# Optimization experiments

Measured on AMD Instinct MI355X. Metric: run time of the kernel, lower is better.

Reference implementation:

```python
import jax, jax.numpy as jnp
import numpy as np

B, T, D, H, C = 256, 512, 300, 128, 6

def setup_inputs() -> dict:
    key = jax.random.key(0)
    ks = jax.random.split(key, 8)
    s = 1.0 / np.sqrt(H)  # PyTorch LSTM/Linear uniform init scale
    x = jax.random.normal(ks[0], (B, T, D), dtype=jnp.float32)
    lengths = jax.random.randint(ks[1], (B,), 1, T + 1)
    W_ih = jax.random.uniform(ks[2], (4 * H, D), minval=-s, maxval=s, dtype=jnp.float32)
    W_hh = jax.random.uniform(ks[3], (4 * H, H), minval=-s, maxval=s, dtype=jnp.float32)
    b_ih = jax.random.uniform(ks[4], (4 * H,), minval=-s, maxval=s, dtype=jnp.float32)
    b_hh = jax.random.uniform(ks[5], (4 * H,), minval=-s, maxval=s, dtype=jnp.float32)
    fc_w = jax.random.uniform(ks[6], (C, H), minval=-s, maxval=s, dtype=jnp.float32)
    fc_b = jax.random.uniform(ks[7], (C,), minval=-s, maxval=s, dtype=jnp.float32)
    return {"x": x, "W_ih": W_ih, "W_hh": W_hh, "b_ih": b_ih, "b_hh": b_hh,
            "fc_w": fc_w, "fc_b": fc_b, "lengths": lengths}

def _lstm_last_hidden(x, W_ih, W_hh, b_ih, b_hh, lengths):
    # Equivalent to pack_padded_sequence + nn.LSTM: the returned hidden[-1]
    # is the state at t = length-1 for each sequence. We run a masked scan:
    # state updates are frozen once t >= length.
    Bv, Tv, _ = x.shape
    Hv = W_hh.shape[1]
    xs = jnp.swapaxes(x, 0, 1)                              # [T, B, D]
    gx = jnp.einsum('tbd,gd->tbg', xs, W_ih) + b_ih + b_hh  # [T, B, 4H]
    mask = (jnp.arange(Tv)[:, None] < lengths[None, :])     # [T, B]

    def step(carry, inp):
        h, c = carry
        g, m = inp
        gates = g + h @ W_hh.T                              # [B, 4H]
        i, f, gg, o = jnp.split(gates, 4, axis=-1)          # PyTorch gate order i,f,g,o
        i = jax.nn.sigmoid(i)
        f = jax.nn.sigmoid(f)
        gg = jnp.tanh(gg)
        o = jax.nn.sigmoid(o)
        c_new = f * c + i * gg
        h_new = o * jnp.tanh(c_new)
        m = m[:, None]
        h = jnp.where(m, h_new, h)
        c = jnp.where(m, c_new, c)
        return (h, c), None

    h0 = jnp.zeros((Bv, Hv), dtype=x.dtype)
    c0 = jnp.zeros((Bv, Hv), dtype=x.dtype)
    (h, c), _ = jax.lax.scan(step, (h0, c0), (gx, mask))
    return h

def reference(x, W_ih, W_hh, b_ih, b_hh, fc_w, fc_b, lengths):
    h = _lstm_last_hidden(x, W_ih, W_hh, b_ih, b_hh, lengths)  # [B, H]
    return h @ fc_w.T + fc_b                                   # [B, 6]
```

## Files before the change

kernel.cpp:

```cpp
#include <hip/hip_runtime.h>
#include <hip/hip_bf16.h>
#include <stdint.h>
#include <type_traits>

#define NB 256
#define NT 512
#define ND 300
#define NH 128
#define NG 512
#define NC 6

typedef __attribute__((ext_vector_type(8))) short short8;
typedef __attribute__((ext_vector_type(4))) float f32x4;

static __device__ __forceinline__ float bf2f(unsigned int u) {
  return __builtin_bit_cast(float, (u & 0xffffu) << 16);
}
static __device__ __forceinline__ unsigned short f2bf(float f) {
  return __builtin_bit_cast(unsigned short, __float2bfloat16(f));
}
static __device__ __forceinline__ unsigned int packbf(float a, float b) {
  return (unsigned int)f2bf(a) | ((unsigned int)f2bf(b) << 16);
}
static __device__ __forceinline__ float ld1(const unsigned short* p) { return bf2f(*p); }
static __device__ __forceinline__ float ld1(const float* p) { return *p; }
static __device__ __forceinline__ void st1(unsigned short* p, float v) { *p = f2bf(v); }
static __device__ __forceinline__ void st1(float* p, float v) { *p = v; }

static __device__ __forceinline__ float sigmoid_fast(float x) {
  return __builtin_amdgcn_rcpf(1.f + __expf(-x));
}
static __device__ __forceinline__ float tanh_fast(float x) {
  return 1.f - 2.f * __builtin_amdgcn_rcpf(__expf(2.f * x) + 1.f);
}

#define BARRIER_LGKM() asm volatile("s_waitcnt lgkmcnt(0)\n\ts_barrier" ::: "memory")

static __device__ __forceinline__ uint2 load4bf_fast(const unsigned short* row, int k) {
  return *(const uint2*)(row + k);
}
static __device__ __forceinline__ uint2 load4bf_fast(const float* row, int k) {
  float4 f = *(const float4*)(row + k);
  uint2 v;
  v.x = packbf(f.x, f.y);
  v.y = packbf(f.z, f.w);
  return v;
}
static __device__ __forceinline__ uint2 load4bf(const unsigned short* row, int k, int lim) {
  if (k + 3 < lim) return load4bf_fast(row, k);
  unsigned int e0 = (k + 0 < lim) ? row[k + 0] : 0;
  unsigned int e1 = (k + 1 < lim) ? row[k + 1] : 0;
  unsigned int e2 = (k + 2 < lim) ? row[k + 2] : 0;
  unsigned int e3 = (k + 3 < lim) ? row[k + 3] : 0;
  uint2 v;
  v.x = e0 | (e1 << 16);
  v.y = e2 | (e3 << 16);
  return v;
}
static __device__ __forceinline__ uint2 load4bf(const float* row, int k, int lim) {
  if (k + 3 < lim) return load4bf_fast(row, k);
  float f0 = (k + 0 < lim) ? row[k + 0] : 0.f;
  float f1 = (k + 1 < lim) ? row[k + 1] : 0.f;
  float f2 = (k + 2 < lim) ? row[k + 2] : 0.f;
  float f3 = (k + 3 < lim) ? row[k + 3] : 0.f;
  uint2 v;
  v.x = packbf(f0, f1);
  v.y = packbf(f2, f3);
  return v;
}

static __device__ __forceinline__ int block_detect(const unsigned short* __restrict__ X,
                                                   int* cnt) {
  const int tid = threadIdx.x;
  const int nthr = blockDim.x;
  if (tid == 0) *cnt = 0;
  __syncthreads();
  int c = 0;
  for (int i = tid; i < 512; i += nthr) {
    unsigned int u = X[i];
    unsigned int e = (u >> 7) & 0xffu;
    if (u == 0u || (e >= 97u && e <= 157u)) c++;
  }
  if (c) atomicAdd(cnt, c);
  __syncthreads();
  return (*cnt >= 448) ? 0 : 1;
}

template <typename XT, typename GXT>
static __device__ __forceinline__ void gx_body(
    const XT* __restrict__ X, const XT* __restrict__ Wih,
    const XT* __restrict__ bih, const XT* __restrict__ bhh,
    const int* __restrict__ lengths, GXT* __restrict__ gx,
    int b_base, int t_base, int Tc, unsigned short* smem) {
  auto As = reinterpret_cast<unsigned short(*)[64][40]>(smem);
  auto Bs = reinterpret_cast<unsigned short(*)[128][40]>(smem + 25600);

  const int mb = blockIdx.x;
  const int m0 = mb << 6;
  const int bc = m0 / Tc;
  const int trel0 = m0 % Tc;
  const int b = b_base + bc;
  const int t0 = t_base + trel0;
  const int len = lengths[b];
  if (t0 >= len) return;

  const int tid = threadIdx.x;
  const int lane = tid & 63;
  const int wave = tid >> 6;
  const int wm = wave & 1;
  const int wn = wave >> 1;
  const int lq = lane >> 4;
  const int lr = lane & 15;

  const int rA = tid >> 2;
  const int cA = (tid & 3) << 2;
  const XT* xrow = X + ((size_t)b * NT + t0 + rA) * ND;
  {
    uint2 a0[10], a1[10];
#pragma unroll
    for (int kc = 0; kc < 9; ++kc) {
      a0[kc] = load4bf_fast(xrow, kc * 32 + cA);
      a1[kc] = load4bf_fast(xrow, kc * 32 + 16 + cA);
    }
    a0[9] = load4bf(xrow, 288 + cA, ND);
    a1[9] = load4bf(xrow, 288 + 16 + cA, ND);
#pragma unroll
    for (int kc = 0; kc < 10; ++kc) {
      *(uint2*)&As[kc][rA][cA] = a0[kc];
      *(uint2*)&As[kc][rA][16 + cA] = a1[kc];
    }
  }

  const int rb = tid >> 3;
  const int kq = tid & 7;

  uint2 bv[3][4];
  {
    const XT* wb = Wih + (size_t)rb * ND;
#pragma unroll
    for (int s3 = 0; s3 < 3; ++s3)
#pragma unroll
      for (int j = 0; j < 4; ++j)
        bv[s3][j] = load4bf_fast(wb + (size_t)(32 * j) * ND, s3 * 32 + kq * 4);
  }

  for (int nt = 0; nt < 4; ++nt) {
    const int n0 = nt << 7;
    const XT* wb = Wih + (size_t)(n0 + rb) * ND;

    f32x4 acc[2][4];
#pragma unroll
    for (int i = 0; i < 2; ++i)
#pragma unroll
      for (int j = 0; j < 4; ++j) {
        f32x4 z = {0.f, 0.f, 0.f, 0.f};
        acc[i][j] = z;
      }

#pragma unroll
    for (int j = 0; j < 4; ++j) *(uint2*)&Bs[0][rb + 32 * j][kq * 4] = bv[0][j];
    BARRIER_LGKM();

#pragma unroll
    for (int kc = 0; kc < 10; ++kc) {
      const int bi = kc & 1;
      if (kc < 9) {
#pragma unroll
        for (int j = 0; j < 4; ++j)
          *(uint2*)&Bs[bi ^ 1][rb + 32 * j][kq * 4] = bv[(kc + 1) % 3][j];
      }
      if (kc < 7) {
        const int kn = (kc + 3) * 32 + kq * 4;
        if (kc < 6) {
#pragma unroll
          for (int j = 0; j < 4; ++j)
            bv[kc % 3][j] = load4bf_fast(wb + (size_t)(32 * j) * ND, kn);
        } else {
#pragma unroll
          for (int j = 0; j < 4; ++j)
            bv[kc % 3][j] = load4bf(wb + (size_t)(32 * j) * ND, kn, ND);
        }
      }

      short8 af[2], bq[4];
#pragma unroll
      for (int tm = 0; tm < 2; ++tm)
        af[tm] = *(const short8*)&As[kc][wm * 32 + tm * 16 + lr][lq * 8];
#pragma unroll
      for (int tn = 0; tn < 4; ++tn)
        bq[tn] = *(const short8*)&Bs[bi][wn * 64 + tn * 16 + lr][lq * 8];
#pragma unroll
      for (int tm = 0; tm < 2; ++tm)
#pragma unroll
        for (int tn = 0; tn < 4; ++tn)
          acc[tm][tn] =
              __builtin_amdgcn_mfma_f32_16x16x32_bf16(af[tm], bq[tn], acc[tm][tn], 0, 0, 0);
      BARRIER_LGKM();
    }

    if (nt < 3) {
      const XT* wb2 = Wih + (size_t)((nt + 1) * 128 + rb) * ND;
#pragma unroll
      for (int s3 = 0; s3 < 3; ++s3)
#pragma unroll
        for (int j = 0; j < 4; ++j)
          bv[s3][j] = load4bf_fast(wb2 + (size_t)(32 * j) * ND, s3 * 32 + kq * 4);
    }

    float bias_c[4];
#pragma unroll
    for (int tn = 0; tn < 4; ++tn) {
      const int col = n0 + wn * 64 + tn * 16 + lr;
      bias_c[tn] = ld1(bih + col) + ld1(bhh + col);
    }
#pragma unroll
    for (int tm = 0; tm < 2; ++tm)
#pragma unroll
      for (int tn = 0; tn < 4; ++tn)
#pragma unroll
        for (int rg = 0; rg < 4; ++rg) {
          const int row = wm * 32 + tm * 16 + lq * 4 + rg;
          if (t0 + row < len) {
            const int col = n0 + wn * 64 + tn * 16 + lr;
            st1(gx + (size_t)(m0 + row) * NG + col, acc[tm][tn][rg] + bias_c[tn]);
          }
        }
  }
}

template <typename XT, typename GXT>
static __device__ __forceinline__ void rec_body(
    const GXT* __restrict__ gx, const XT* __restrict__ Whh,
    const XT* __restrict__ fcw, const XT* __restrict__ fcb,
    const int* __restrict__ lengths, XT* __restrict__ out,
    float* __restrict__ hstate, float* __restrict__ cstate,
    int b_base, int t_base, int Tc,
    unsigned short (*hpk)[NH], float* hf) {
  const int bc = blockIdx.x;
  const int b = b_base + bc;
  int len = lengths[b];
  if (len > NT) len = NT;
  if (len < 0) len = 0;
  const bool first = (t_base == 0);
  const bool last = (t_base + Tc >= NT);
  const int tend = (len < t_base + Tc) ? len : (t_base + Tc);
  if (!last && tend <= t_base) return;
  int nsteps = tend - t_base;
  if (nsteps < 0) nsteps = 0;

  const int tid = threadIdx.x;
  const int w8 = tid >> 6;
  const int l = tid & 63;
  const int q = l >> 4;
  const int m = l & 15;
  const int u0 = w8 * 16 + q * 4;
  const int r = m & 3;
  const int u = u0 + r;

  short8 afr[4][4];
#pragma unroll
  for (int g = 0; g < 4; ++g) {
    const int row = g * NH + w8 * 16 + m;
    if constexpr (std::is_same_v<XT, unsigned short>) {
#pragma unroll
      for (int c = 0; c < 4; ++c)
        afr[g][c] = *(const short8*)(Whh + (size_t)row * NH + c * 32 + q * 8);
    } else {
#pragma unroll
      for (int c = 0; c < 4; ++c) {
        const float* p = Whh + (size_t)row * NH + c * 32 + q * 8;
        float4 f0 = *(const float4*)p;
        float4 f1 = *(const float4*)(p + 4);
        union { unsigned int uu[4]; short8 s; } cv2;
        cv2.uu[0] = packbf(f0.x, f0.y);
        cv2.uu[1] = packbf(f0.z, f0.w);
        cv2.uu[2] = packbf(f1.x, f1.y);
        cv2.uu[3] = packbf(f1.z, f1.w);
        afr[g][c] = cv2.s;
      }
    }
  }

  float hcur = 0.f, ccur = 0.f;
  if (!first) {
    hcur = hstate[(size_t)bc * NH + u];
    ccur = cstate[(size_t)bc * NH + u];
  }
  if (m < 4) hpk[0][u] = f2bf(hcur);
  __syncthreads();

  const GXT* gp = gx + (size_t)bc * Tc * NG + u;
  const int lastidx = (nsteps > 0) ? nsteps - 1 : 0;

  float gs0[4], gs1[4];
  {
    const int i1 = (1 < lastidx) ? 1 : lastidx;
#pragma unroll
    for (int g = 0; g < 4; ++g) {
      gs0[g] = ld1(gp + g * NH);
      gs1[g] = ld1(gp + (size_t)i1 * NG + g * NH);
    }
  }

#define REC_STEP(S, PAR, GC)                                                         \
  {                                                                                  \
    short8 bfr[4];                                                                   \
    const unsigned short* hrow = hpk[(PAR)];                                         \
    _Pragma("unroll") for (int c = 0; c < 4; ++c)                                    \
        bfr[c] = *(const short8*)&hrow[c * 32 + q * 8];                              \
    const f32x4 zz = {0.f, 0.f, 0.f, 0.f};                                           \
    f32x4 acc[4];                                                                    \
    _Pragma("unroll") for (int g = 0; g < 4; ++g) {                                  \
      f32x4 p0 = __builtin_amdgcn_mfma_f32_16x16x32_bf16(afr[g][0], bfr[0], zz, 0, 0, 0); \
      f32x4 p1 = __builtin_amdgcn_mfma_f32_16x16x32_bf16(afr[g][1], bfr[1], zz, 0, 0, 0); \
      f32x4 p2 = __builtin_amdgcn_mfma_f32_16x16x32_bf16(afr[g][2], bfr[2], zz, 0, 0, 0); \
      f32x4 p3 = __builtin_amdgcn_mfma_f32_16x16x32_bf16(afr[g][3], bfr[3], zz, 0, 0, 0); \
      acc[g] = (p0 + p1) + (p2 + p3);                                                \
    }                                                                                \
    float pre[4];                                                                    \
    _Pragma("unroll") for (int g = 0; g < 4; ++g) {                                  \
      const float t0v = (r & 1) ? acc[g][1] : acc[g][0];                             \
      const float t1v = (r & 1) ? acc[g][3] : acc[g][2];                             \
      pre[g] = ((r & 2) ? t1v : t0v) + GC[g];                                        \
    }                                                                                \
    {                                                                                \
      int idx_ = (S) + 2;                                                            \
      if (idx_ > lastidx) idx_ = lastidx;                                            \
      _Pragma("unroll") for (int g = 0; g < 4; ++g)                                  \
          GC[g] = ld1(gp + (size_t)idx_ * NG + g * NH);                              \
    }                                                                                \
    const float ig = sigmoid_fast(pre[0]);                                           \
    const float fg = sigmoid_fast(pre[1]);                                           \
    const float gg = tanh_fast(pre[2]);                                              \
    const float og = sigmoid_fast(pre[3]);                                           \
    ccur = fmaf(fg, ccur, ig * gg);                                                  \
    hcur = og * tanh_fast(ccur);                                                     \
    if (m < 4) hpk[(PAR) ^ 1][u] = f2bf(hcur);                                       \
    BARRIER_LGKM();                                                                  \
  }

  int s = 0;
  for (; s + 1 < nsteps; s += 2) {
    REC_STEP(s, 0, gs0);
    REC_STEP(s + 1, 1, gs1);
  }
  if (s < nsteps) {
    REC_STEP(s, 0, gs0);
  }
#undef REC_STEP

  if (!last) {
    if (m < 4) {
      hstate[(size_t)bc * NH + u] = hcur;
      cstate[(size_t)bc * NH + u] = ccur;
    }
  } else {
    if (m < 4) hf[u] = hcur;
    __syncthreads();
    if (tid < NC) {
      float acc = ld1(fcb + tid);
      const XT* wv = fcw + (size_t)tid * NH;
#pragma unroll
      for (int k = 0; k < NH; ++k) acc = fmaf(ld1(wv + k), hf[k], acc);
      st1(out + (size_t)b * NC + tid, acc);
    }
  }
}

template <typename GXT>
__global__ __launch_bounds__(256) void gx_gemm_rt(const void* __restrict__ X,
                                                  const void* __restrict__ Wih,
                                                  const void* __restrict__ bih,
                                                  const void* __restrict__ bhh,
                                                  const int* __restrict__ lengths,
                                                  GXT* __restrict__ gx,
                                                  int b_base, int t_base, int Tc) {
  __shared__ int cnt;
  __shared__ __align__(16) unsigned short smem[35840];
  const int isf32 = block_detect((const unsigned short*)X, &cnt);
  if (isf32)
    gx_body<float, GXT>((const float*)X, (const float*)Wih, (const float*)bih,
                        (const float*)bhh, lengths, gx, b_base, t_base, Tc, smem);
  else
    gx_body<unsigned short, GXT>((const unsigned short*)X, (const unsigned short*)Wih,
                                 (const unsigned short*)bih, (const unsigned short*)bhh,
                                 lengths, gx, b_base, t_base, Tc, smem);
}

template <typename GXT>
__global__ __launch_bounds__(512)
__attribute__((amdgpu_waves_per_eu(2, 2)))
void lstm_rec_rt(const void* __restrict__ X, const GXT* __restrict__ gx,
                 const void* __restrict__ Whh, const void* __restrict__ fcw,
                 const void* __restrict__ fcb, const int* __restrict__ lengths,
                 void* __restrict__ out, float* __restrict__ hstate,
                 float* __restrict__ cstate, int b_base, int t_base, int Tc) {
  __shared__ int cnt;
  __shared__ __align__(16) unsigned short hpk[2][NH];
  __shared__ __align__(16) float hf[NH];
  const int isf32 = block_detect((const unsigned short*)X, &cnt);
  if (isf32)
    rec_body<float, GXT>(gx, (const float*)Whh, (const float*)fcw, (const float*)fcb,
                         lengths, (float*)out, hstate, cstate, b_base, t_base, Tc,
                         hpk, hf);
  else
    rec_body<unsigned short, GXT>(gx, (const unsigned short*)Whh,
                                  (const unsigned short*)fcw,
                                  (const unsigned short*)fcb, lengths,
                                  (unsigned short*)out, hstate, cstate, b_base,
                                  t_base, Tc, hpk, hf);
}

template <typename GXT>
static void run_all(void* const* d_in, void* d_out, GXT* gx, float* hstate,
                    float* cstate, int NBc, int Tc, hipStream_t stream) {
  const int* lengths = (const int*)d_in[7];
  for (int bb = 0; bb < NB; bb += NBc) {
    for (int tb = 0; tb < NT; tb += Tc) {
      gx_gemm_rt<GXT><<<dim3((NBc * Tc) / 64), dim3(256), 0, stream>>>(
          d_in[0], d_in[1], d_in[3], d_in[4], lengths, gx, bb, tb, Tc);
      lstm_rec_rt<GXT><<<dim3(NBc), dim3(512), 0, stream>>>(
          d_in[0], gx, d_in[2], d_in[5], d_in[6], lengths, d_out, hstate, cstate,
          bb, tb, Tc);
    }
  }
}

extern "C" void kernel_launch(void* const* d_in, const int* in_sizes, int n_in,
                              void* d_out, int out_size, void* d_ws, size_t ws_size,
                              hipStream_t stream) {
  const size_t full_f32 = (size_t)NB * NT * NG * sizeof(float);
  const size_t full_bf16 = (size_t)NB * NT * NG * 2;
  const size_t base = 512;

  int NBc, Tc;
  char* gx_raw;
  float* hstate = (float*)((char*)d_ws + base);
  bool gx_is_f32;

  if (ws_size >= base + full_f32) {
    NBc = NB; Tc = NT; gx_is_f32 = true;
    gx_raw = (char*)d_ws + base;
  } else if (ws_size >= base + full_bf16) {
    NBc = NB; Tc = NT; gx_is_f32 = false;
    gx_raw = (char*)d_ws + base;
  } else {
    Tc = 128; gx_is_f32 = false;
    NBc = 1;
    for (int cand : {64, 16, 4}) {
      size_t need = base + (size_t)cand * NH * 2 * sizeof(float) + (size_t)cand * Tc * NG * 2;
      if (ws_size >= need) { NBc = cand; break; }
    }
    gx_raw = (char*)d_ws + base + (size_t)NBc * NH * 2 * sizeof(float);
  }
  float* cstate = hstate + (size_t)NBc * NH;

  if (gx_is_f32) {
    run_all<float>(d_in, d_out, (float*)gx_raw, hstate, cstate, NBc, Tc, stream);
  } else {
    run_all<unsigned short>(d_in, d_out, (unsigned short*)gx_raw, hstate, cstate,
                            NBc, Tc, stream);
  }
}
```

Measured before the change: 710.3 us.

## Widen gx GEMM blocks to 512 threads with transposed MFMA and vectorized stores

The input-projection GEMM now runs with 512 threads per block, each wave covering a 32x32 output tile instead of 32x64. Operands are swapped in the MFMA so each lane holds four consecutive gate columns, which lets the epilogue write gx as one 16-byte (or packed bf16) store instead of scalar stores. The recurrent step drops the four partial-sum MFMAs plus adds in favour of a chained accumulation. This aims for better memory coalescing and latency hiding in the GEMM, at the cost of more per-block register and barrier pressure and a longer MFMA dependency chain in the recurrence.

```diff
diff --git a/kernel.cpp b/kernel.cpp
--- a/kernel.cpp
+++ b/kernel.cpp
@@ -87,144 +87,194 @@
 }
 
 template <typename XT, typename GXT>
-static __device__ __forceinline__ void gx_body(
+static __device__ __forceinline__ void gx_prod(
     const XT* __restrict__ X, const XT* __restrict__ Wih,
     const XT* __restrict__ bih, const XT* __restrict__ bhh,
-    const int* __restrict__ lengths, GXT* __restrict__ gx,
-    int b_base, int t_base, int Tc, unsigned short* smem) {
+    int b, int t0, int len, GXT* __restrict__ gxrow, unsigned short* smem) {
   auto As = reinterpret_cast<unsigned short(*)[64][40]>(smem);
   auto Bs = reinterpret_cast<unsigned short(*)[128][40]>(smem + 25600);
-
-  const int mb = blockIdx.x;
-  const int m0 = mb << 6;
-  const int bc = m0 / Tc;
-  const int trel0 = m0 % Tc;
-  const int b = b_base + bc;
-  const int t0 = t_base + trel0;
-  const int len = lengths[b];
-  if (t0 >= len) return;
 
   const int tid = threadIdx.x;
   const int lane = tid & 63;
   const int wave = tid >> 6;
-  const int wm = wave & 1;
-  const int wn = wave >> 1;
+  const int wt = wave & 1;
+  const int wn4 = wave >> 1;
   const int lq = lane >> 4;
   const int lr = lane & 15;
 
-  const int rA = tid >> 2;
-  const int cA = (tid & 3) << 2;
+  const int rA = tid >> 3;
+  const int cA = (tid & 7) << 2;
   const XT* xrow = X + ((size_t)b * NT + t0 + rA) * ND;
   {
-    uint2 a0[10], a1[10];
-#pragma unroll
-    for (int kc = 0; kc < 9; ++kc) {
-      a0[kc] = load4bf_fast(xrow, kc * 32 + cA);
-      a1[kc] = load4bf_fast(xrow, kc * 32 + 16 + cA);
-    }
-    a0[9] = load4bf(xrow, 288 + cA, ND);
-    a1[9] = load4bf(xrow, 288 + 16 + cA, ND);
-#pragma unroll
-    for (int kc = 0; kc < 10; ++kc) {
-      *(uint2*)&As[kc][rA][cA] = a0[kc];
-      *(uint2*)&As[kc][rA][16 + cA] = a1[kc];
-    }
-  }
-
-  const int rb = tid >> 3;
-  const int kq = tid & 7;
-
-  uint2 bv[3][4];
+    uint2 a[10];
+#pragma unroll
+    for (int kc = 0; kc < 9; ++kc) a[kc] = load4bf_fast(xrow, kc * 32 + cA);
+    a[9] = load4bf(xrow, 288 + cA, ND);
+#pragma unroll
+    for (int kc = 0; kc < 10; ++kc) *(uint2*)&As[kc][rA][cA] = a[kc];
+  }
+
+  const int rb = tid >> 2;
+  const int kqo = (tid & 3) << 3;
+  uint2 bv[3][2];
   {
     const XT* wb = Wih + (size_t)rb * ND;
 #pragma unroll
-    for (int s3 = 0; s3 < 3; ++s3)
-#pragma unroll
-      for (int j = 0; j < 4; ++j)
-        bv[s3][j] = load4bf_fast(wb + (size_t)(32 * j) * ND, s3 * 32 + kq * 4);
+    for (int s3 = 0; s3 < 3; ++s3) {
+      bv[s3][0] = load4bf_fast(wb, s3 * 32 + kqo);
+      bv[s3][1] = load4bf_fast(wb, s3 * 32 + kqo + 4);
+    }
   }
 
   for (int nt = 0; nt < 4; ++nt) {
     const int n0 = nt << 7;
     const XT* wb = Wih + (size_t)(n0 + rb) * ND;
 
-    f32x4 acc[2][4];
+    f32x4 acc[2][2];
 #pragma unroll
     for (int i = 0; i < 2; ++i)
 #pragma unroll
-      for (int j = 0; j < 4; ++j) {
+      for (int j = 0; j < 2; ++j) {
         f32x4 z = {0.f, 0.f, 0.f, 0.f};
         acc[i][j] = z;
       }
 
-#pragma unroll
-    for (int j = 0; j < 4; ++j) *(uint2*)&Bs[0][rb + 32 * j][kq * 4] = bv[0][j];
+    *(uint2*)&Bs[0][rb][kqo] = bv[0][0];
+    *(uint2*)&Bs[0][rb][kqo + 4] = bv[0][1];
     BARRIER_LGKM();
 
 #pragma unroll
     for (int kc = 0; kc < 10; ++kc) {
       const int bi = kc & 1;
       if (kc < 9) {
-#pragma unroll
-        for (int j = 0; j < 4; ++j)
-          *(uint2*)&Bs[bi ^ 1][rb + 32 * j][kq * 4] = bv[(kc + 1) % 3][j];
+        *(uint2*)&Bs[bi ^ 1][rb][kqo] = bv[(kc + 1) % 3][0];
+        *(uint2*)&Bs[bi ^ 1][rb][kqo + 4] = bv[(kc + 1) % 3][1];
       }
       if (kc < 7) {
-        const int kn = (kc + 3) * 32 + kq * 4;
+        const int kn = (kc + 3) * 32 + kqo;
         if (kc < 6) {
-#pragma unroll
-          for (int j = 0; j < 4; ++j)
-            bv[kc % 3][j] = load4bf_fast(wb + (size_t)(32 * j) * ND, kn);
+          bv[kc % 3][0] = load4bf_fast(wb, kn);
+          bv[kc % 3][1] = load4bf_fast(wb, kn + 4);
         } else {
-#pragma unroll
-          for (int j = 0; j < 4; ++j)
-            bv[kc % 3][j] = load4bf(wb + (size_t)(32 * j) * ND, kn, ND);
+          bv[kc % 3][0] = load4bf(wb, kn, ND);
+          bv[kc % 3][1] = load4bf(wb, kn + 4, ND);
         }
       }
 
-      short8 af[2], bq[4];
-#pragma unroll
-      for (int tm = 0; tm < 2; ++tm)
-        af[tm] = *(const short8*)&As[kc][wm * 32 + tm * 16 + lr][lq * 8];
-#pragma unroll
-      for (int tn = 0; tn < 4; ++tn)
-        bq[tn] = *(const short8*)&Bs[bi][wn * 64 + tn * 16 + lr][lq * 8];
-#pragma unroll
-      for (int tm = 0; tm < 2; ++tm)
-#pragma unroll
-        for (int tn = 0; tn < 4; ++tn)
-          acc[tm][tn] =
-              __builtin_amdgcn_mfma_f32_16x16x32_bf16(af[tm], bq[tn], acc[tm][tn], 0, 0, 0);
+      short8 wF[2], aX[2];
+#pragma unroll
+      for (int tn = 0; tn < 2; ++tn)
+        wF[tn] = *(const short8*)&Bs[bi][wn4 * 32 + tn * 16 + lr][lq * 8];
+#pragma unroll
+      for (int tt = 0; tt < 2; ++tt)
+        aX[tt] = *(const short8*)&As[kc][wt * 32 + tt * 16 + lr][lq * 8];
+#pragma unroll
+      for (int tt = 0; tt < 2; ++tt)
+#pragma unroll
+        for (int tn = 0; tn < 2; ++tn)
+          acc[tt][tn] =
+              __builtin_amdgcn_mfma_f32_16x16x32_bf16(wF[tn], aX[tt], acc[tt][tn], 0, 0, 0);
       BARRIER_LGKM();
     }
 
     if (nt < 3) {
       const XT* wb2 = Wih + (size_t)((nt + 1) * 128 + rb) * ND;
 #pragma unroll
-      for (int s3 = 0; s3 < 3; ++s3)
-#pragma unroll
-        for (int j = 0; j < 4; ++j)
-          bv[s3][j] = load4bf_fast(wb2 + (size_t)(32 * j) * ND, s3 * 32 + kq * 4);
-    }
-
-    float bias_c[4];
-#pragma unroll
-    for (int tn = 0; tn < 4; ++tn) {
-      const int col = n0 + wn * 64 + tn * 16 + lr;
-      bias_c[tn] = ld1(bih + col) + ld1(bhh + col);
-    }
-#pragma unroll
-    for (int tm = 0; tm < 2; ++tm)
-#pragma unroll
-      for (int tn = 0; tn < 4; ++tn)
-#pragma unroll
-        for (int rg = 0; rg < 4; ++rg) {
-          const int row = wm * 32 + tm * 16 + lq * 4 + rg;
-          if (t0 + row < len) {
-            const int col = n0 + wn * 64 + tn * 16 + lr;
-            st1(gx + (size_t)(m0 + row) * NG + col, acc[tm][tn][rg] + bias_c[tn]);
+      for (int s3 = 0; s3 < 3; ++s3) {
+        bv[s3][0] = load4bf_fast(wb2, s3 * 32 + kqo);
+        bv[s3][1] = load4bf_fast(wb2, s3 * 32 + kqo + 4);
+      }
+    }
+
+    f32x4 bias4[2];
+#pragma unroll
+    for (int tn = 0; tn < 2; ++tn) {
+      const int n = n0 + wn4 * 32 + tn * 16 + lq * 4;
+#pragma unroll
+      for (int rg = 0; rg < 4; ++rg) bias4[tn][rg] = ld1(bih + n + rg) + ld1(bhh + n + rg);
+    }
+#pragma unroll
+    for (int tt = 0; tt < 2; ++tt) {
+      const int trow = wt * 32 + tt * 16 + lr;
+      if (t0 + trow < len) {
+#pragma unroll
+        for (int tn = 0; tn < 2; ++tn) {
+          const int n = n0 + wn4 * 32 + tn * 16 + lq * 4;
+          f32x4 o = acc[tt][tn] + bias4[tn];
+          if constexpr (std::is_same_v<GXT, float>) {
+            *(f32x4*)(gxrow + (size_t)trow * NG + n) = o;
+          } else {
+            uint2 v;
+            v.x = packbf(o[0], o[1]);
+            v.y = packbf(o[2], o[3]);
+            *(uint2*)(gxrow + (size_t)trow * NG + n) = v;
           }
         }
+      }
+    }
+  }
+}
+
+#define REC_STEP(S, PAR, GC, CAP)                                                    \
+  {                                                                                  \
+    short8 bfr[4];                                                                   \
+    const unsigned short* hrow = hpk[(PAR)];                                         \
+    _Pragma("unroll") for (int c = 0; c < 4; ++c)                                    \
+        bfr[c] = *(const short8*)&hrow[c * 32 + q * 8];                              \
+    f32x4 acc[4];                                                                    \
+    _Pragma("unroll") for (int g = 0; g < 4; ++g) {                                  \
+      f32x4 z = {0.f, 0.f, 0.f, 0.f};                                                \
+      acc[g] = z;                                                                    \
+      _Pragma("unroll") for (int c = 0; c < 4; ++c)                                  \
+          acc[g] = __builtin_amdgcn_mfma_f32_16x16x32_bf16(afr[g][c], bfr[c],        \
+                                                           acc[g], 0, 0, 0);         \
+    }                                                                                \
+    float pre[4];                                                                    \
+    _Pragma("unroll") for (int g = 0; g < 4; ++g) {                                  \
+      const float t0v = (r & 1) ? acc[g][1] : acc[g][0];                             \
+      const float t1v = (r & 1) ? acc[g][3] : acc[g][2];                             \
+      pre[g] = ((r & 2) ? t1v : t0v) + GC[g];                                        \
+    }                                                                                \
+    {                                                                                \
+      int idx_ = (S) + 2;                                                            \
+      if (idx_ > (CAP)) idx_ = (CAP);                                                \
+      _Pragma("unroll") for (int g = 0; g < 4; ++g)                                  \
+          GC[g] = ld1(gp + (size_t)idx_ * NG + g * NH);                              \
+    }                                                                                \
+    const float ig = sigmoid_fast(pre[0]);                                           \
+    const float fg = sigmoid_fast(pre[1]);                                           \
+    const float gg = tanh_fast(pre[2]);                                              \
+    const float og = sigmoid_fast(pre[3]);                                           \
+    ccur = fmaf(fg, ccur, ig * gg);                                                  \
+    hcur = og * tanh_fast(ccur);                                                     \
+    if (m < 4) hpk[(PAR) ^ 1][u] = f2bf(hcur);                                       \
+    BARRIER_LGKM();                                                                  \
+  }
+
+template <typename XT>
+static __device__ __forceinline__ void load_afr(const XT* __restrict__ Whh, int w8,
+                                                int q, int m, short8 afr[4][4]) {
+#pragma unroll
+  for (int g = 0; g < 4; ++g) {
+    const int row = g * NH + w8 * 16 + m;
+    if constexpr (std::is_same_v<XT, unsigned short>) {
+#pragma unroll
+      for (int c = 0; c < 4; ++c)
+        afr[g][c] = *(const short8*)(Whh + (size_t)row * NH + c * 32 + q * 8);
+    } else {
+#pragma unroll
+      for (int c = 0; c < 4; ++c) {
+        const float* p = Whh + (size_t)row * NH + c * 32 + q * 8;
+        float4 f0 = *(const float4*)p;
+        float4 f1 = *(const float4*)(p + 4);
+        union { unsigned int uu[4]; short8 s; } cv2;
+        cv2.uu[0] = packbf(f0.x, f0.y);
+        cv2.uu[1] = packbf(f0.z, f0.w);
+        cv2.uu[2] = packbf(f1.x, f1.y);
+        cv2.uu[3] = packbf(f1.z, f1.w);
+        afr[g][c] = cv2.s;
+      }
+    }
   }
 }
 
@@ -258,28 +308,7 @@
   const int u = u0 + r;
 
   short8 afr[4][4];
-#pragma unroll
-  for (int g = 0; g < 4; ++g) {
-    const int row = g * NH + w8 * 16 + m;
-    if constexpr (std::is_same_v<XT, unsigned short>) {
-#pragma unroll
-      for (int c = 0; c < 4; ++c)
-        afr[g][c] = *(const short8*)(Whh + (size_t)row * NH + c * 32 + q * 8);
-    } else {
-#pragma unroll
-      for (int c = 0; c < 4; ++c) {
-        const float* p = Whh + (size_t)row * NH + c * 32 + q * 8;
-        float4 f0 = *(const float4*)p;
-        float4 f1 = *(const float4*)(p + 4);
-        union { unsigned int uu[4]; short8 s; } cv2;
-        cv2.uu[0] = packbf(f0.x, f0.y);
-        cv2.uu[1] = packbf(f0.z, f0.w);
-        cv2.uu[2] = packbf(f1.x, f1.y);
-        cv2.uu[3] = packbf(f1.z, f1.w);
-        afr[g][c] = cv2.s;
-      }
-    }
-  }
+  load_afr<XT>(Whh, w8, q, m, afr);
 
   float hcur = 0.f, ccur = 0.f;
   if (!first) {
@@ -302,52 +331,14 @@
     }
   }
 
-#define REC_STEP(S, PAR, GC)                                                         \
-  {                                                                                  \
-    short8 bfr[4];                                                                   \
-    const unsigned short* hrow = hpk[(PAR)];                                         \
-    _Pragma("unroll") for (int c = 0; c < 4; ++c)                                    \
-        bfr[c] = *(const short8*)&hrow[c * 32 + q * 8];                              \
-    const f32x4 zz = {0.f, 0.f, 0.f, 0.f};                                           \
-    f32x4 acc[4];                                                                    \
-    _Pragma("unroll") for (int g = 0; g < 4; ++g) {                                  \
-      f32x4 p0 = __builtin_amdgcn_mfma_f32_16x16x32_bf16(afr[g][0], bfr[0], zz, 0, 0, 0); \
-      f32x4 p1 = __builtin_amdgcn_mfma_f32_16x16x32_bf16(afr[g][1], bfr[1], zz, 0, 0, 0); \
-      f32x4 p2 = __builtin_amdgcn_mfma_f32_16x16x32_bf16(afr[g][2], bfr[2], zz, 0, 0, 0); \
-      f32x4 p3 = __builtin_amdgcn_mfma_f32_16x16x32_bf16(afr[g][3], bfr[3], zz, 0, 0, 0); \
-      acc[g] = (p0 + p1) + (p2 + p3);                                                \
-    }                                                                                \
-    float pre[4];                                                                    \
-    _Pragma("unroll") for (int g = 0; g < 4; ++g) {                                  \
-      const float t0v = (r & 1) ? acc[g][1] : acc[g][0];                             \
-      const float t1v = (r & 1) ? acc[g][3] : acc[g][2];                             \
-      pre[g] = ((r & 2) ? t1v : t0v) + GC[g];                                        \
-    }                                                                                \
-    {                                                                                \
-      int idx_ = (S) + 2;                                                            \
-      if (idx_ > lastidx) idx_ = lastidx;                                            \
-      _Pragma("unroll") for (int g = 0; g < 4; ++g)                                  \
-          GC[g] = ld1(gp + (size_t)idx_ * NG + g * NH);                              \
-    }                                                                                \
-    const float ig = sigmoid_fast(pre[0]);                                           \
-    const float fg = sigmoid_fast(pre[1]);                                           \
-    const float gg = tanh_fast(pre[2]);                                              \
-    const float og = sigmoid_fast(pre[3]);                                           \
-    ccur = fmaf(fg, ccur, ig * gg);                                                  \
-    hcur = og * tanh_fast(ccur);                                                     \
-    if (m < 4) hpk[(PAR) ^ 1][u] = f2bf(hcur);                                       \
-    BARRIER_LGKM();                                                                  \
-  }
-
   int s = 0;
   for (; s + 1 < nsteps; s += 2) {
-    REC_STEP(s, 0, gs0);
-    REC_STEP(s + 1, 1, gs1);
+    REC_STEP(s, 0, gs0, lastidx);
+    REC_STEP(s + 1, 1, gs1, lastidx);
   }
   if (s < nsteps) {
-    REC_STEP(s, 0, gs0);
-  }
-#undef REC_STEP
+    REC_STEP(s, 0, gs0, lastidx);
+  }
 
   if (!last) {
     if (m < 4) {
@@ -368,23 +359,32 @@
 }
 
 template <typename GXT>
-__global__ __launch_bounds__(256) void gx_gemm_rt(const void* __restrict__ X,
-                                                  const void* __restrict__ Wih,
-                                                  const void* __restrict__ bih,
-                                                  const void* __restrict__ bhh,
-                                                  const int* __restrict__ lengths,
-                                                  GXT* __restrict__ gx,
-                                                  int b_base, int t_base, int Tc) {
+__global__ __launch_bounds__(512, 4) void gx_gemm_rt(const void* __restrict__ X,
+                                                     const void* __restrict__ Wih,
+                                                     const void* __restrict__ bih,
+                                                     const void* __restrict__ bhh,
+                                                     const int* __restrict__ lengths,
+                                                     GXT* __restrict__ gx,
+                                                     int b_base, int t_base, int Tc) {
   __shared__ int cnt;
   __shared__ __align__(16) unsigned short smem[35840];
   const int isf32 = block_detect((const unsigned short*)X, &cnt);
+  const int m0 = blockIdx.x << 6;
+  const int bc = m0 / Tc;
+  const int trel = m0 % Tc;
+  const int b = b_base + bc;
+  const int t0 = t_base + trel;
+  int len = lengths[b];
+  if (len > NT) len = NT;
+  if (t0 >= len) return;
+  GXT* gxrow = gx + (size_t)m0 * NG;
   if (isf32)
-    gx_body<float, GXT>((const float*)X, (const float*)Wih, (const float*)bih,
-                        (const float*)bhh, lengths, gx, b_base, t_base, Tc, smem);
+    gx_prod<float, GXT>((const float*)X, (const float*)Wih, (const float*)bih,
+                        (const float*)bhh, b, t0, len, gxrow, smem);
   else
-    gx_body<unsigned short, GXT>((const unsigned short*)X, (const unsigned short*)Wih,
+    gx_prod<unsigned short, GXT>((const unsigned short*)X, (const unsigned short*)Wih,
                                  (const unsigned short*)bih, (const unsigned short*)bhh,
-                                 lengths, gx, b_base, t_base, Tc, smem);
+                                 b, t0, len, gxrow, smem);
 }
 
 template <typename GXT>
@@ -417,7 +417,7 @@
   const int* lengths = (const int*)d_in[7];
   for (int bb = 0; bb < NB; bb += NBc) {
     for (int tb = 0; tb < NT; tb += Tc) {
-      gx_gemm_rt<GXT><<<dim3((NBc * Tc) / 64), dim3(256), 0, stream>>>(
+      gx_gemm_rt<GXT><<<dim3((NBc * Tc) / 64), dim3(512), 0, stream>>>(
           d_in[0], d_in[1], d_in[3], d_in[4], lengths, gx, bb, tb, Tc);
       lstm_rec_rt<GXT><<<dim3(NBc), dim3(512), 0, stream>>>(
           d_in[0], gx, d_in[2], d_in[5], d_in[6], lengths, d_out, hstate, cstate,
```

Measured after the change: 580.0 us. -18.3%, faster.
